# Kernel optimization log

Hardware: AMD Instinct MI355X
Metric: run time of the kernel (lower is better)

The kernel has to match this reference:

```python
import jax, jax.numpy as jnp
import numpy as np

# ----- ESPRIT constants (mirror the torch module's __init__ defaults / init_kwargs) -----
FS = 16000
N_FFT = 512
HOP = 256
C_SOUND = 343.0
D_INTER = 0.08
SRC_NUM = 2
MIC_NUM = 4
F_LOW = 400.0
F_HIGH = 1000.0
EST_NUM = 4      # get_spt_mat(X, 4, 120)
T_START = 120


def setup_inputs() -> dict:
    """Synthesize 2 broadband plane-wave sources hitting a 4-mic ULA.

    Pure white noise per channel would make asin(phase*c/(2*pi*f*d)) leave
    [-1, 1] (NaNs). Physically delayed sources keep the ESPRIT math well-posed.
    """
    T = 1_920_000  # 2 minutes @ 16 kHz
    rng = np.random.default_rng(0)
    s = rng.standard_normal((SRC_NUM, T))
    thetas = np.deg2rad(np.array([20.0, -40.0]))               # source DOAs
    taus = (np.arange(MIC_NUM)[None, :] * D_INTER
            * np.sin(thetas)[:, None] / C_SOUND)              # (S, M) delays
    f = np.fft.rfftfreq(T, d=1.0 / FS)                        # (T//2+1,)
    S = np.fft.rfft(s, axis=-1)                               # (S, F)
    x = np.zeros((T, MIC_NUM))
    for i in range(SRC_NUM):
        # exact circular fractional delay per mic, in the frequency domain
        shifted = np.fft.irfft(S[i][None, :]
                               * np.exp(-2j * np.pi * f[None, :] * taus[i][:, None]),
                               n=T, axis=-1)                   # (M, T)
        x += shifted.T
    x += 1e-4 * rng.standard_normal((T, MIC_NUM))              # sensor noise
    return {"x": jnp.asarray(x, dtype=jnp.float32)}


def _stft(x):
    """x: (C, T) -> (C, F, T_frames). Matches torch.stft defaults:
    center=True, pad_mode='reflect', onesided=True, window=sqrt(hann_periodic)."""
    n = jnp.arange(N_FFT)
    win = jnp.sqrt(0.5 - 0.5 * jnp.cos(2.0 * jnp.pi * n / N_FFT)).astype(x.dtype)
    pad = N_FFT // 2
    xp = jnp.pad(x, ((0, 0), (pad, pad)), mode='reflect')
    n_frames = (xp.shape[-1] - N_FFT) // HOP + 1
    idx = jnp.arange(n_frames)[:, None] * HOP + jnp.arange(N_FFT)[None, :]
    frames = xp[:, idx] * win                      # (C, n_frames, n_fft)
    return jnp.fft.rfft(frames, axis=-1).transpose(0, 2, 1)  # (C, F, n_frames)


# static frequency-bin selection (shapes must be static under jit)
_FA = np.linspace(0.0, FS / 2, N_FFT // 2 + 1)
_USE_IDX = np.nonzero((_FA >= F_LOW) & (_FA < F_HIGH))[0]   # 19 bins


def _forward(x):
    X = _stft(x.T)                                  # (C, F, Tf)
    f_use = jnp.asarray(_FA[_USE_IDX], dtype=jnp.float32)      # (Fb,)
    Xs = X[:, _USE_IDX, T_START:T_START + EST_NUM]  # (C, Fb, E)
    # spatial covariance: spt[f] = mean_t x_f(t) x_f(t)^H  -> (Fb, M, M)
    spt = jnp.einsum('mft,nft->fmn', Xs, jnp.conj(Xs)) / EST_NUM
    # signal subspace = top-SRC_NUM eigenvectors (batched Hermitian eig)
    _, V = jnp.linalg.eigh(spt)                     # ascending eigenvalues
    sig = V[..., ::-1][..., :SRC_NUM]               # (Fb, M, S) dominant
    s0, s1 = sig[:, :-1, :], sig[:, 1:, :]          # (Fb, M-1, S)
    # phi = pinv(s0) @ s1 = (s0^H s0)^{-1} s0^H s1  (full column rank)
    A = jnp.einsum('fmi,fmj->fij', jnp.conj(s0), s0)
    B = jnp.einsum('fmi,fmj->fij', jnp.conj(s0), s1)
    phi = jnp.linalg.solve(A, B)                    # (Fb, 2, 2)
    # closed-form eigenvalues of batched 2x2 complex matrices
    tr = phi[..., 0, 0] + phi[..., 1, 1]
    det = phi[..., 0, 0] * phi[..., 1, 1] - phi[..., 0, 1] * phi[..., 1, 0]
    disc = jnp.sqrt(tr * tr - 4.0 * det)
    lam = jnp.stack([(tr + disc) * 0.5, (tr - disc) * 0.5], axis=-1)  # (Fb, 2)
    phase = jnp.arctan2(lam.imag, lam.real)
    ang = jnp.degrees(jnp.arcsin(phase * C_SOUND
                                 / (2.0 * jnp.pi * f_use[:, None] * D_INTER)))
    return jnp.mean(ang)                            # scalar DOA estimate


def reference(x):
    return _forward(x)
```

## Files before the change

### kernel.cpp

```cpp
#include <hip/hip_runtime.h>
#include <math.h>


#define NFFT   512
#define KLO    13
#define NK     19
#define NTT    4
#define NMIC   4
#define XBASE  30464
#define PI_F   3.14159265358979f

#define FRM_STRIDE 2084
#define CHK_STRIDE 260
#define XW_SIZE    8328

struct cf { float x, y; };
__device__ inline cf cadd(cf a, cf b){ return {a.x+b.x, a.y+b.y}; }
__device__ inline cf csub(cf a, cf b){ return {a.x-b.x, a.y-b.y}; }
__device__ inline cf cmul(cf a, cf b){ return {a.x*b.x - a.y*b.y, a.x*b.y + a.y*b.x}; }
__device__ inline cf cmulc(cf a, cf b){ return {a.x*b.x + a.y*b.y, a.y*b.x - a.x*b.y}; }
__device__ inline cf cscale(cf a, float s){ return {a.x*s, a.y*s}; }
__device__ inline cf csqrtf_c(cf z){
    float r = sqrtf(z.x*z.x + z.y*z.y);
    float u = sqrtf(fmaxf(0.5f*(r + z.x), 0.0f));
    float v = sqrtf(fmaxf(0.5f*(r - z.x), 0.0f));
    if (z.y < 0.0f) v = -v;
    return {u, v};
}

__global__ __launch_bounds__(640)
void esprit_kernel(const float* __restrict__ x, float* __restrict__ out)
{
    __shared__ __align__(16) float xw[XW_SIZE];
    __shared__ float XsR[NK][NTT][NMIC], XsI[NK][NTT][NMIC];

    const int tid = threadIdx.x;

    for (int e = tid; e < NTT * NFFT; e += 640) {
        int t = e >> 9;
        int n = e & 511;
        float4 v = ((const float4*)x)[XBASE + t * 256 + n];
        float w = __sinf((float)n * (PI_F / 512.0f));
        v.x *= w; v.y *= w; v.z *= w; v.w *= w;
        *(float4*)&xw[t * FRM_STRIDE + (n >> 6) * CHK_STRIDE + (n & 63) * 4] = v;
    }
    __syncthreads();

    if (tid < 608) {
        const int bin = tid >> 3;
        const int p   = tid & 7;
        const int kk  = bin >> 2;
        const int t   = bin & 3;
        const int k   = KLO + kk;
        const int n0  = p << 6;
        const int j0  = (k * n0) & 511;

        float cr, ci, wc, ws;
        __sincosf((float)j0 * (-2.0f * PI_F / 512.0f), &ci, &cr);
        __sincosf((float)k  * (-2.0f * PI_F / 512.0f), &ws, &wc);

        float re0=0,re1=0,re2=0,re3=0, im0=0,im1=0,im2=0,im3=0;
        const int boff = t * FRM_STRIDE + p * CHK_STRIDE;
        #pragma unroll 8
        for (int i = 0; i < 64; ++i) {
            float4 v = *(const float4*)&xw[boff + 4*i];
            re0 = fmaf(v.x, cr, re0); im0 = fmaf(v.x, ci, im0);
            re1 = fmaf(v.y, cr, re1); im1 = fmaf(v.y, ci, im1);
            re2 = fmaf(v.z, cr, re2); im2 = fmaf(v.z, ci, im2);
            re3 = fmaf(v.w, cr, re3); im3 = fmaf(v.w, ci, im3);
            float nr = fmaf(cr, wc, -(ci * ws));
            float ni = fmaf(cr, ws,  (ci * wc));
            cr = nr; ci = ni;
        }
        #pragma unroll
        for (int mask = 1; mask < 8; mask <<= 1) {
            re0 += __shfl_xor(re0, mask); im0 += __shfl_xor(im0, mask);
            re1 += __shfl_xor(re1, mask); im1 += __shfl_xor(im1, mask);
            re2 += __shfl_xor(re2, mask); im2 += __shfl_xor(im2, mask);
            re3 += __shfl_xor(re3, mask); im3 += __shfl_xor(im3, mask);
        }
        if (p == 0) {
            XsR[kk][t][0] = re0; XsI[kk][t][0] = im0;
            XsR[kk][t][1] = re1; XsI[kk][t][1] = im1;
            XsR[kk][t][2] = re2; XsI[kk][t][2] = im2;
            XsR[kk][t][3] = re3; XsI[kk][t][3] = im3;
        }
    }
    __syncthreads();

    float asum = 0.0f;
    if (tid < 64) {
        if (tid < NK) {
            cf Xm[NMIC][NTT];
            for (int m = 0; m < NMIC; ++m)
                for (int t = 0; t < NTT; ++t)
                    Xm[m][t] = { XsR[tid][t][m], XsI[tid][t][m] };

            cf R[4][4];
            for (int i = 0; i < 4; ++i)
                for (int j = 0; j < 4; ++j) {
                    cf acc = {0.f, 0.f};
                    for (int t = 0; t < 4; ++t) acc = cadd(acc, cmulc(Xm[i][t], Xm[j][t]));
                    R[i][j] = cscale(acc, 0.25f);
                }

            cf Q[4][2], Y[4][2];
            for (int i = 0; i < 4; ++i) { Y[i][0] = R[i][0]; Y[i][1] = R[i][1]; }
            float nrm0 = 0.f;
            for (int i = 0; i < 4; ++i) nrm0 += Y[i][0].x*Y[i][0].x + Y[i][0].y*Y[i][0].y;
            float in0 = __builtin_amdgcn_rsqf(nrm0);
            for (int i = 0; i < 4; ++i) Q[i][0] = cscale(Y[i][0], in0);
            cf pr = {0.f, 0.f};
            for (int i = 0; i < 4; ++i) pr = cadd(pr, cmulc(Y[i][1], Q[i][0]));
            for (int i = 0; i < 4; ++i) Q[i][1] = csub(Y[i][1], cmul(pr, Q[i][0]));
            float nrm1 = 0.f;
            for (int i = 0; i < 4; ++i) nrm1 += Q[i][1].x*Q[i][1].x + Q[i][1].y*Q[i][1].y;
            float in1 = __builtin_amdgcn_rsqf(nrm1);
            for (int i = 0; i < 4; ++i) Q[i][1] = cscale(Q[i][1], in1);

            float a00 = 0.f, a11 = 0.f;
            cf a01 = {0.f, 0.f};
            cf B[2][2] = { { {0,0}, {0,0} }, { {0,0}, {0,0} } };
            for (int i = 0; i < 3; ++i) {
                a00 += Q[i][0].x*Q[i][0].x + Q[i][0].y*Q[i][0].y;
                a11 += Q[i][1].x*Q[i][1].x + Q[i][1].y*Q[i][1].y;
                a01 = cadd(a01, cmulc(Q[i][1], Q[i][0]));
                for (int r2 = 0; r2 < 2; ++r2)
                    for (int c2 = 0; c2 < 2; ++c2)
                        B[r2][c2] = cadd(B[r2][c2], cmulc(Q[i+1][c2], Q[i][r2]));
            }
            float detA = a00*a11 - (a01.x*a01.x + a01.y*a01.y);
            float inv  = __builtin_amdgcn_rcpf(detA);
            cf na01  = { -a01.x, -a01.y };
            cf na01c = { -a01.x,  a01.y };
            cf phi00 = cscale(cadd(cscale(B[0][0], a11), cmul(na01,  B[1][0])), inv);
            cf phi01 = cscale(cadd(cscale(B[0][1], a11), cmul(na01,  B[1][1])), inv);
            cf phi10 = cscale(cadd(cmul(na01c, B[0][0]), cscale(B[1][0], a00)), inv);
            cf phi11 = cscale(cadd(cmul(na01c, B[0][1]), cscale(B[1][1], a00)), inv);

            cf tr = cadd(phi00, phi11);
            cf dt = csub(cmul(phi00, phi11), cmul(phi01, phi10));
            cf d2 = csub(cmul(tr, tr), cscale(dt, 4.0f));
            cf disc = csqrtf_c(d2);
            cf lam0 = cscale(cadd(tr, disc), 0.5f);
            cf lam1 = cscale(csub(tr, disc), 0.5f);

            float f     = 31.25f * (float)(KLO + tid);
            float scale = 343.0f / (2.0f * PI_F * f * 0.08f);
            float ph0 = atan2f(lam0.y, lam0.x);
            float ph1 = atan2f(lam1.y, lam1.x);
            float g0 = fminf(fmaxf(ph0 * scale, -1.0f), 1.0f);
            float g1 = fminf(fmaxf(ph1 * scale, -1.0f), 1.0f);
            asum = (asinf(g0) + asinf(g1)) * (180.0f / PI_F);
        }
        #pragma unroll
        for (int mask = 32; mask >= 1; mask >>= 1)
            asum += __shfl_xor(asum, mask);
        if (tid == 0) out[0] = asum * (1.0f / 38.0f);
    }
}

extern "C" void kernel_launch(void* const* d_in, const int* in_sizes, int n_in,
                              void* d_out, int out_size, void* d_ws, size_t ws_size,
                              hipStream_t stream)
{
    const float* x = (const float*)d_in[0];
    float* out = (float*)d_out;
    esprit_kernel<<<1, 640, 0, stream>>>(x, out);
}
```

Baseline: 11.50 us.

## Compute two DFT bins per thread with 16-way frame split per wave

Restructures the DFT stage so each wave handles two adjacent frequency bins, and each lane processes a 32-sample chunk for both bins. Every shared-memory load of windowed samples is reused for two bins, and the serial loop length is halved. The cost is a longer shuffle reduction (16 lanes instead of 8), twice the accumulator registers, and one padded dummy bin computed by the last wave. The shared-memory chunk stride is changed to match the new split.

```diff
diff --git a/kernel.cpp b/kernel.cpp
--- a/kernel.cpp
+++ b/kernel.cpp
@@ -10,9 +10,9 @@
 #define XBASE  30464
 #define PI_F   3.14159265358979f
 
-#define FRM_STRIDE 2084
-#define CHK_STRIDE 260
-#define XW_SIZE    8328
+#define FRM_STRIDE 2116
+#define CHK_STRIDE 132
+#define XW_SIZE    8456
 
 struct cf { float x, y; };
 __device__ inline cf cadd(cf a, cf b){ return {a.x+b.x, a.y+b.y}; }
@@ -32,7 +32,7 @@
 void esprit_kernel(const float* __restrict__ x, float* __restrict__ out)
 {
     __shared__ __align__(16) float xw[XW_SIZE];
-    __shared__ float XsR[NK][NTT][NMIC], XsI[NK][NTT][NMIC];
+    __shared__ float XsR[NK + 1][NTT][NMIC], XsI[NK + 1][NTT][NMIC];
 
     const int tid = threadIdx.x;
 
@@ -42,48 +42,67 @@
         float4 v = ((const float4*)x)[XBASE + t * 256 + n];
         float w = __sinf((float)n * (PI_F / 512.0f));
         v.x *= w; v.y *= w; v.z *= w; v.w *= w;
-        *(float4*)&xw[t * FRM_STRIDE + (n >> 6) * CHK_STRIDE + (n & 63) * 4] = v;
+        *(float4*)&xw[t * FRM_STRIDE + (n >> 5) * CHK_STRIDE + (n & 31) * 4] = v;
     }
     __syncthreads();
 
-    if (tid < 608) {
-        const int bin = tid >> 3;
-        const int p   = tid & 7;
-        const int kk  = bin >> 2;
-        const int t   = bin & 3;
-        const int k   = KLO + kk;
-        const int n0  = p << 6;
-        const int j0  = (k * n0) & 511;
+    {
+        const int w    = tid >> 6;
+        const int lane = tid & 63;
+        const int t    = lane >> 4;
+        const int p    = lane & 15;
+        const int kk0  = w << 1;
+        const int k0   = KLO + kk0;
+        const int k1   = k0 + 1;
+        const int n0   = p << 5;
 
-        float cr, ci, wc, ws;
-        __sincosf((float)j0 * (-2.0f * PI_F / 512.0f), &ci, &cr);
-        __sincosf((float)k  * (-2.0f * PI_F / 512.0f), &ws, &wc);
+        float cr0, ci0, wc0, ws0, cr1, ci1, wc1, ws1;
+        __sincosf((float)((k0 * n0) & 511) * (-2.0f * PI_F / 512.0f), &ci0, &cr0);
+        __sincosf((float)k0               * (-2.0f * PI_F / 512.0f), &ws0, &wc0);
+        __sincosf((float)((k1 * n0) & 511) * (-2.0f * PI_F / 512.0f), &ci1, &cr1);
+        __sincosf((float)k1               * (-2.0f * PI_F / 512.0f), &ws1, &wc1);
 
-        float re0=0,re1=0,re2=0,re3=0, im0=0,im1=0,im2=0,im3=0;
+        float ar0=0,ar1=0,ar2=0,ar3=0, ai0=0,ai1=0,ai2=0,ai3=0;
+        float br0=0,br1=0,br2=0,br3=0, bi0=0,bi1=0,bi2=0,bi3=0;
         const int boff = t * FRM_STRIDE + p * CHK_STRIDE;
         #pragma unroll 8
-        for (int i = 0; i < 64; ++i) {
+        for (int i = 0; i < 32; ++i) {
             float4 v = *(const float4*)&xw[boff + 4*i];
-            re0 = fmaf(v.x, cr, re0); im0 = fmaf(v.x, ci, im0);
-            re1 = fmaf(v.y, cr, re1); im1 = fmaf(v.y, ci, im1);
-            re2 = fmaf(v.z, cr, re2); im2 = fmaf(v.z, ci, im2);
-            re3 = fmaf(v.w, cr, re3); im3 = fmaf(v.w, ci, im3);
-            float nr = fmaf(cr, wc, -(ci * ws));
-            float ni = fmaf(cr, ws,  (ci * wc));
-            cr = nr; ci = ni;
+            ar0 = fmaf(v.x, cr0, ar0); ai0 = fmaf(v.x, ci0, ai0);
+            ar1 = fmaf(v.y, cr0, ar1); ai1 = fmaf(v.y, ci0, ai1);
+            ar2 = fmaf(v.z, cr0, ar2); ai2 = fmaf(v.z, ci0, ai2);
+            ar3 = fmaf(v.w, cr0, ar3); ai3 = fmaf(v.w, ci0, ai3);
+            br0 = fmaf(v.x, cr1, br0); bi0 = fmaf(v.x, ci1, bi0);
+            br1 = fmaf(v.y, cr1, br1); bi1 = fmaf(v.y, ci1, bi1);
+            br2 = fmaf(v.z, cr1, br2); bi2 = fmaf(v.z, ci1, bi2);
+            br3 = fmaf(v.w, cr1, br3); bi3 = fmaf(v.w, ci1, bi3);
+            float n0r = fmaf(cr0, wc0, -(ci0 * ws0));
+            float n0i = fmaf(cr0, ws0,  (ci0 * wc0));
+            cr0 = n0r; ci0 = n0i;
+            float n1r = fmaf(cr1, wc1, -(ci1 * ws1));
+            float n1i = fmaf(cr1, ws1,  (ci1 * wc1));
+            cr1 = n1r; ci1 = n1i;
         }
         #pragma unroll
-        for (int mask = 1; mask < 8; mask <<= 1) {
-            re0 += __shfl_xor(re0, mask); im0 += __shfl_xor(im0, mask);
-            re1 += __shfl_xor(re1, mask); im1 += __shfl_xor(im1, mask);
-            re2 += __shfl_xor(re2, mask); im2 += __shfl_xor(im2, mask);
-            re3 += __shfl_xor(re3, mask); im3 += __shfl_xor(im3, mask);
+        for (int mask = 1; mask < 16; mask <<= 1) {
+            ar0 += __shfl_xor(ar0, mask); ai0 += __shfl_xor(ai0, mask);
+            ar1 += __shfl_xor(ar1, mask); ai1 += __shfl_xor(ai1, mask);
+            ar2 += __shfl_xor(ar2, mask); ai2 += __shfl_xor(ai2, mask);
+            ar3 += __shfl_xor(ar3, mask); ai3 += __shfl_xor(ai3, mask);
+            br0 += __shfl_xor(br0, mask); bi0 += __shfl_xor(bi0, mask);
+            br1 += __shfl_xor(br1, mask); bi1 += __shfl_xor(bi1, mask);
+            br2 += __shfl_xor(br2, mask); bi2 += __shfl_xor(bi2, mask);
+            br3 += __shfl_xor(br3, mask); bi3 += __shfl_xor(bi3, mask);
         }
         if (p == 0) {
-            XsR[kk][t][0] = re0; XsI[kk][t][0] = im0;
-            XsR[kk][t][1] = re1; XsI[kk][t][1] = im1;
-            XsR[kk][t][2] = re2; XsI[kk][t][2] = im2;
-            XsR[kk][t][3] = re3; XsI[kk][t][3] = im3;
+            XsR[kk0][t][0] = ar0; XsI[kk0][t][0] = ai0;
+            XsR[kk0][t][1] = ar1; XsI[kk0][t][1] = ai1;
+            XsR[kk0][t][2] = ar2; XsI[kk0][t][2] = ai2;
+            XsR[kk0][t][3] = ar3; XsI[kk0][t][3] = ai3;
+            XsR[kk0+1][t][0] = br0; XsI[kk0+1][t][0] = bi0;
+            XsR[kk0+1][t][1] = br1; XsI[kk0+1][t][1] = bi1;
+            XsR[kk0+1][t][2] = br2; XsI[kk0+1][t][2] = bi2;
+            XsR[kk0+1][t][3] = br3; XsI[kk0+1][t][3] = bi3;
         }
     }
     __syncthreads();
```

Measured after the change: 12.81 us. 11.4% more time.
